# Performance work log

Hardware: AMD Instinct MI355X
Metric: run time of the kernel (lower is better)

Reference implementation:

```python
import jax, jax.numpy as jnp
import numpy as np

N_NODES = 50000
N_EDGES = 800000
F_IN = 512
H1 = 64
H2 = 128
N_CLASSES = 10
N_GRAPHS = 64


def _sage_conv(x, src, dst, w_l, b_l, w_r, n_nodes):
    # mean-aggregate neighbor features (messages flow src -> dst), then
    # out = lin_l(mean_neigh) + lin_r(x)   (PyG SAGEConv defaults)
    msg = x[src]                                           # [E, F] gather
    agg = jax.ops.segment_sum(msg, dst, num_segments=n_nodes)
    deg = jax.ops.segment_sum(jnp.ones((src.shape[0], 1), x.dtype), dst,
                              num_segments=n_nodes)
    mean = agg / jnp.maximum(deg, 1.0)                     # 0 for isolated nodes
    return mean @ w_l + b_l + x @ w_r


def setup_inputs() -> dict:
    key = jax.random.key(0)
    ks = jax.random.split(key, 12)
    x = jax.random.normal(ks[0], (N_NODES, F_IN), dtype=jnp.float32)
    edge_index = jax.random.randint(ks[1], (2, N_EDGES), 0, N_NODES, dtype=jnp.int64)
    batch = jnp.sort(jax.random.randint(ks[2], (N_NODES,), 0, N_GRAPHS, dtype=jnp.int64))

    def glorot(k, fan_in, fan_out):
        s = jnp.sqrt(6.0 / (fan_in + fan_out)).astype(jnp.float32)
        return jax.random.uniform(k, (fan_in, fan_out), jnp.float32, -s, s)

    return {
        "x": x, "edge_index": edge_index, "batch": batch,
        "w1_l": glorot(ks[3], F_IN, H1), "b1_l": jnp.zeros((H1,), jnp.float32),
        "w1_r": glorot(ks[4], F_IN, H1),
        "w2_l": glorot(ks[5], H1, H2), "b2_l": jnp.zeros((H2,), jnp.float32),
        "w2_r": glorot(ks[6], H1, H2),
        "w_fc": glorot(ks[7], H2, N_CLASSES),
        "b_fc": jnp.zeros((N_CLASSES,), jnp.float32),
    }


def reference(x, edge_index, batch, w1_l, b1_l, w1_r, w2_l, b2_l, w2_r, w_fc, b_fc):
    src, dst = edge_index[0], edge_index[1]
    n = x.shape[0]
    h = jax.nn.relu(_sage_conv(x, src, dst, w1_l, b1_l, w1_r, n))
    # dropout is identity in eval mode
    h = _sage_conv(h, src, dst, w2_l, b2_l, w2_r, n)        # [N, H2]
    # global mean pool over graphs
    summed = jax.ops.segment_sum(h, batch, num_segments=N_GRAPHS)
    cnt = jax.ops.segment_sum(jnp.ones((n, 1), h.dtype), batch, num_segments=N_GRAPHS)
    pooled = summed / jnp.maximum(cnt, 1.0)                 # [G, H2]
    logits = pooled @ w_fc + b_fc                           # [G, C]
    return jax.nn.log_softmax(logits, axis=1)
```

## Files before the change

### kernel.cpp

```cpp
#include <hip/hip_runtime.h>

#define NN 50000
#define NE 800000
#define FIN 512
#define H1DIM 64
#define H2DIM 128
#define NC 10
#define NG 64
#define NRT 3125
#define SCAN_BLOCKS 196

typedef __attribute__((ext_vector_type(8))) short bf16x8;
typedef __attribute__((ext_vector_type(4))) float f32x4;

__device__ inline short f2bf(float f) {
  unsigned u = __float_as_uint(f);
  unsigned r = u + 0x7fffu + ((u >> 16) & 1u);
  return (short)(r >> 16);
}
__device__ inline float bf2f(short s) {
  return __uint_as_float(((unsigned)(unsigned short)s) << 16);
}

__global__ __launch_bounds__(256) void hist_kernel(const int* __restrict__ dst,
                                                   int* __restrict__ cnt) {
  int i = (blockIdx.x * 256 + threadIdx.x) * 4;
  if (i < NE) {
    int4 d = *(const int4*)(dst + i);
    atomicAdd(&cnt[d.x], 1);
    atomicAdd(&cnt[d.y], 1);
    atomicAdd(&cnt[d.z], 1);
    atomicAdd(&cnt[d.w], 1);
  }
}

__global__ __launch_bounds__(256) void scan1_kernel(const int* __restrict__ cnt,
                                                    int* __restrict__ excl,
                                                    int* __restrict__ bsum) {
  __shared__ int s[256];
  int t = threadIdx.x;
  int i = blockIdx.x * 256 + t;
  int v = (i < NN) ? cnt[i] : 0;
  s[t] = v;
  __syncthreads();
  for (int off = 1; off < 256; off <<= 1) {
    int u = (t >= off) ? s[t - off] : 0;
    __syncthreads();
    s[t] += u;
    __syncthreads();
  }
  if (i < NN) excl[i] = s[t] - v;
  if (t == 255) bsum[blockIdx.x] = s[255];
}

__global__ __launch_bounds__(256) void scan23_kernel(const int* __restrict__ bsum,
                                                     int* __restrict__ rowptr,
                                                     int* __restrict__ cursor) {
  __shared__ int s[256];
  int t = threadIdx.x;
  int b = blockIdx.x;
  int v = (t < SCAN_BLOCKS) ? bsum[t] : 0;
  s[t] = v;
  __syncthreads();
  for (int off = 1; off < 256; off <<= 1) {
    int u = (t >= off) ? s[t - off] : 0;
    __syncthreads();
    s[t] += u;
    __syncthreads();
  }
  int prefix = (b == 0) ? 0 : s[b - 1];
  int i = b * 256 + t;
  if (i < NN) {
    int p = rowptr[i] + prefix;
    rowptr[i] = p;
    cursor[i] = p;
  }
  if (i == 0) rowptr[NN] = NE;
}

__global__ __launch_bounds__(256) void scatter_kernel(
    const int* __restrict__ src, const int* __restrict__ dst,
    int* __restrict__ cursor, int* __restrict__ ssrc) {
  int i = (blockIdx.x * 256 + threadIdx.x) * 4;
  if (i < NE) {
    int4 s = *(const int4*)(src + i);
    int4 d = *(const int4*)(dst + i);
    int p0 = atomicAdd(&cursor[d.x], 1); ssrc[p0] = s.x;
    int p1 = atomicAdd(&cursor[d.y], 1); ssrc[p1] = s.y;
    int p2 = atomicAdd(&cursor[d.z], 1); ssrc[p2] = s.z;
    int p3 = atomicAdd(&cursor[d.w], 1); ssrc[p3] = s.w;
  }
}

__global__ __launch_bounds__(256) void wbtf_prep_kernel(
    const float* __restrict__ wl, const float* __restrict__ wr,
    short* __restrict__ wbtf) {
  int w = blockIdx.x * 4 + (threadIdx.x >> 6);
  int lane = threadIdx.x & 63;
  int ni = w >> 4;
  int ks = w & 15;
  int n = ni * 16 + (lane & 15);
  int k = ks * 32 + (lane >> 4) * 8;
  bf16x8 o;
#pragma unroll
  for (int j = 0; j < 8; j++) {
    float v = (n < 64) ? wl[(size_t)(k + j) * 64 + n]
                       : wr[(size_t)(k + j) * 64 + (n - 64)];
    o[j] = f2bf(v);
  }
  *(bf16x8*)(wbtf + ((size_t)w * 64 + lane) * 8) = o;
}

__global__ __launch_bounds__(256) void gemm1_kernel(
    const float* __restrict__ x, const short* __restrict__ wbtf,
    short* __restrict__ xwl, float* __restrict__ xwr) {
  int w = blockIdx.x * 4 + (threadIdx.x >> 6);
  if (w >= NRT) return;
  int lane = threadIdx.x & 63;
  int l15 = lane & 15;
  int q = lane >> 4;
  const float* px = x + (size_t)(w * 16 + l15) * FIN + q * 8;
  const short* pb = wbtf + (size_t)lane * 8;

  const f32x4 z = {0.f, 0.f, 0.f, 0.f};
  f32x4 acc[8];
#pragma unroll
  for (int ni = 0; ni < 8; ni++) acc[ni] = z;

  float4 av0, av1, nv0, nv1;
  bf16x8 B0[8], B1[8];
  av0 = *(const float4*)(px);
  av1 = *(const float4*)(px + 4);
#pragma unroll
  for (int ni = 0; ni < 8; ni++)
    B0[ni] = *(const bf16x8*)(pb + (size_t)ni * 8192);

#pragma unroll
  for (int ks = 0; ks < 16; ks += 2) {
    if (ks + 1 < 16) {
      nv0 = *(const float4*)(px + (ks + 1) * 32);
      nv1 = *(const float4*)(px + (ks + 1) * 32 + 4);
#pragma unroll
      for (int ni = 0; ni < 8; ni++)
        B1[ni] = *(const bf16x8*)(pb + (size_t)ni * 8192 + (ks + 1) * 512);
    }
    {
      bf16x8 af;
      af[0] = f2bf(av0.x); af[1] = f2bf(av0.y);
      af[2] = f2bf(av0.z); af[3] = f2bf(av0.w);
      af[4] = f2bf(av1.x); af[5] = f2bf(av1.y);
      af[6] = f2bf(av1.z); af[7] = f2bf(av1.w);
#pragma unroll
      for (int ni = 0; ni < 8; ni++)
        acc[ni] = __builtin_amdgcn_mfma_f32_16x16x32_bf16(af, B0[ni], acc[ni], 0, 0, 0);
    }
    if (ks + 2 < 16) {
      av0 = *(const float4*)(px + (ks + 2) * 32);
      av1 = *(const float4*)(px + (ks + 2) * 32 + 4);
#pragma unroll
      for (int ni = 0; ni < 8; ni++)
        B0[ni] = *(const bf16x8*)(pb + (size_t)ni * 8192 + (ks + 2) * 512);
    }
    {
      bf16x8 af;
      af[0] = f2bf(nv0.x); af[1] = f2bf(nv0.y);
      af[2] = f2bf(nv0.z); af[3] = f2bf(nv0.w);
      af[4] = f2bf(nv1.x); af[5] = f2bf(nv1.y);
      af[6] = f2bf(nv1.z); af[7] = f2bf(nv1.w);
#pragma unroll
      for (int ni = 0; ni < 8; ni++)
        acc[ni] = __builtin_amdgcn_mfma_f32_16x16x32_bf16(af, B1[ni], acc[ni], 0, 0, 0);
    }
  }

  int row_base = w * 16 + q * 4;
#pragma unroll
  for (int ni = 0; ni < 8; ni++) {
    int col = ni * 16 + l15;
    int c = col & 63;
#pragma unroll
    for (int r = 0; r < 4; r++) {
      int row = row_base + r;
      if (col < 64) xwl[(size_t)row * 64 + c] = f2bf(acc[ni][r]);
      else          xwr[(size_t)row * 64 + c] = acc[ni][r];
    }
  }
}

__global__ __launch_bounds__(256) void agg1_h1_kernel(
    const int* __restrict__ rowptr, const int* __restrict__ ssrc,
    const short* __restrict__ xwl, const float* __restrict__ xwr,
    const float* __restrict__ b1, short* __restrict__ h1) {
  int node = blockIdx.x * 4 + (threadIdx.x >> 6);
  if (node >= NN) return;
  int lane = threadIdx.x & 63;
  int c = lane & 7;
  int r = lane >> 3;
  int lo = rowptr[node], hi = rowptr[node + 1];
  float acc[8];
#pragma unroll
  for (int k = 0; k < 8; k++) acc[k] = 0.f;
  for (int e = lo + r; e < hi; e += 8) {
    int s = ssrc[e];
    bf16x8 v = *(const bf16x8*)(xwl + (size_t)s * 64 + c * 8);
#pragma unroll
    for (int k = 0; k < 8; k++) acc[k] += bf2f(v[k]);
  }
#pragma unroll
  for (int k = 0; k < 8; k++) {
    acc[k] += __shfl_xor(acc[k], 8);
    acc[k] += __shfl_xor(acc[k], 16);
    acc[k] += __shfl_xor(acc[k], 32);
  }
  if (r == 0) {
    float dg = fmaxf((float)(hi - lo), 1.0f);
    const float* xr = xwr + (size_t)node * 64 + c * 8;
    bf16x8 out;
#pragma unroll
    for (int k = 0; k < 8; k++) {
      float v = fmaxf(acc[k] / dg + b1[c * 8 + k] + xr[k], 0.f);
      out[k] = f2bf(v);
    }
    *(bf16x8*)(h1 + (size_t)node * 64 + c * 8) = out;
  }
}

__global__ __launch_bounds__(256) void agg2_kernel(
    const int* __restrict__ rowptr, const int* __restrict__ ssrc,
    const short* __restrict__ h1, float* __restrict__ agg2) {
  int node = blockIdx.x * 4 + (threadIdx.x >> 6);
  if (node >= NN) return;
  int lane = threadIdx.x & 63;
  int c = lane & 7;
  int r = lane >> 3;
  int lo = rowptr[node], hi = rowptr[node + 1];
  float acc[8];
#pragma unroll
  for (int k = 0; k < 8; k++) acc[k] = 0.f;
  for (int e = lo + r; e < hi; e += 8) {
    int s = ssrc[e];
    bf16x8 v = *(const bf16x8*)(h1 + (size_t)s * 64 + c * 8);
#pragma unroll
    for (int k = 0; k < 8; k++) acc[k] += bf2f(v[k]);
  }
#pragma unroll
  for (int k = 0; k < 8; k++) {
    acc[k] += __shfl_xor(acc[k], 8);
    acc[k] += __shfl_xor(acc[k], 16);
    acc[k] += __shfl_xor(acc[k], 32);
  }
  if (r == 0) {
    float* p = agg2 + (size_t)node * 64 + c * 8;
    f32x4 lo4 = {acc[0], acc[1], acc[2], acc[3]};
    f32x4 hi4 = {acc[4], acc[5], acc[6], acc[7]};
    *(f32x4*)(p) = lo4;
    *(f32x4*)(p + 4) = hi4;
  }
}

__global__ __launch_bounds__(256) void pool1_kernel(
    const int* __restrict__ batch, const float* __restrict__ agg2,
    const short* __restrict__ h1, const int* __restrict__ rowptr,
    float* __restrict__ poolA, float* __restrict__ poolB,
    float* __restrict__ poolCnt) {
  int t = threadIdx.x;
  int c = t & 15;
  int s = t >> 4;
  int n0 = blockIdx.x * 256 + s * 16;
  int n1 = n0 + 16;
  if (n1 > NN) n1 = NN;

  f32x4 aA = {0.f, 0.f, 0.f, 0.f};
  f32x4 aB = {0.f, 0.f, 0.f, 0.f};
  int cur_g = -1;
  float run = 0.f;
  for (int n = n0; n < n1; n++) {
    int g = batch[n];
    if (g != cur_g) {
      if (cur_g >= 0) {
        float* pa = poolA + (size_t)cur_g * 64 + c * 4;
        float* pb = poolB + (size_t)cur_g * 64 + c * 4;
#pragma unroll
        for (int k = 0; k < 4; k++) {
          atomicAdd(&pa[k], aA[k]);
          atomicAdd(&pb[k], aB[k]);
        }
        if (c == 0) atomicAdd(&poolCnt[cur_g], run);
      }
      cur_g = g;
      aA = (f32x4){0.f, 0.f, 0.f, 0.f};
      aB = (f32x4){0.f, 0.f, 0.f, 0.f};
      run = 0.f;
    }
    float rd = 1.0f / fmaxf((float)(rowptr[n + 1] - rowptr[n]), 1.0f);
    f32x4 a2 = *(const f32x4*)(agg2 + (size_t)n * 64 + c * 4);
    const short* hp = h1 + (size_t)n * 64 + c * 4;
#pragma unroll
    for (int k = 0; k < 4; k++) {
      aA[k] = fmaf(a2[k], rd, aA[k]);
      aB[k] += bf2f(hp[k]);
    }
    run += 1.f;
  }
  if (cur_g >= 0) {
    float* pa = poolA + (size_t)cur_g * 64 + c * 4;
    float* pb = poolB + (size_t)cur_g * 64 + c * 4;
#pragma unroll
    for (int k = 0; k < 4; k++) {
      atomicAdd(&pa[k], aA[k]);
      atomicAdd(&pb[k], aB[k]);
    }
    if (c == 0) atomicAdd(&poolCnt[cur_g], run);
  }
}

__global__ __launch_bounds__(128) void final_kernel(
    const float* __restrict__ poolA, const float* __restrict__ poolB,
    const float* __restrict__ poolCnt, const float* __restrict__ w2l,
    const float* __restrict__ w2r, const float* __restrict__ b2,
    const float* __restrict__ wfc, const float* __restrict__ bfc,
    float* __restrict__ out) {
  int g = blockIdx.x;
  int j = threadIdx.x;
  __shared__ float sp[H2DIM];
  __shared__ float sl[NC];

  float invc = 1.0f / fmaxf(poolCnt[g], 1.0f);
  float v = b2[j];
  for (int k = 0; k < 64; k++) {
    float a = poolA[g * 64 + k] * invc;
    float b = poolB[g * 64 + k] * invc;
    v = fmaf(a, w2l[k * 128 + j], v);
    v = fmaf(b, w2r[k * 128 + j], v);
  }
  sp[j] = v;
  __syncthreads();
  if (j < NC) {
    float lg = bfc[j];
    for (int k = 0; k < H2DIM; k++) lg = fmaf(sp[k], wfc[k * NC + j], lg);
    sl[j] = lg;
  }
  __syncthreads();
  if (j < NC) {
    float m = -1e30f;
    for (int k = 0; k < NC; k++) m = fmaxf(m, sl[k]);
    float s = 0.f;
    for (int k = 0; k < NC; k++) s += expf(sl[k] - m);
    out[g * NC + j] = sl[j] - m - logf(s);
  }
}

extern "C" void kernel_launch(void* const* d_in, const int* in_sizes, int n_in,
                              void* d_out, int out_size, void* d_ws,
                              size_t ws_size, hipStream_t stream) {
  const float* x   = (const float*)d_in[0];
  const int* edge  = (const int*)d_in[1];
  const int* batch = (const int*)d_in[2];
  const float* w1l = (const float*)d_in[3];
  const float* b1l = (const float*)d_in[4];
  const float* w1r = (const float*)d_in[5];
  const float* w2l = (const float*)d_in[6];
  const float* b2l = (const float*)d_in[7];
  const float* w2r = (const float*)d_in[8];
  const float* wfc = (const float*)d_in[9];
  const float* bfc = (const float*)d_in[10];
  float* out = (float*)d_out;

  const int* src = edge;
  const int* dst = edge + NE;

  const size_t NF = (size_t)NN * 64;
  int*   cnt     = (int*)d_ws;
  float* poolA   = (float*)(cnt + NN);
  float* poolB   = poolA + (size_t)NG * 64;
  float* poolCnt = poolB + (size_t)NG * 64;
  int*   cursor  = (int*)(poolCnt + NG);
  int*   rowptr  = cursor + NN;
  int*   bsum    = rowptr + 50004;
  int*   ssrc    = bsum + 256;
  short* xwl     = (short*)(ssrc + NE);
  short* h1s     = xwl + NF;
  short* wbtf    = h1s + NF;
  float* xwr     = (float*)(wbtf + 65536);
  float* agg2    = xwr + NF;

  hipMemsetAsync(cnt, 0, (NN + 2 * NG * 64 + NG) * sizeof(int), stream);

  hist_kernel<<<(NE / 4 + 255) / 256, 256, 0, stream>>>(dst, cnt);
  scan1_kernel<<<SCAN_BLOCKS, 256, 0, stream>>>(cnt, rowptr, bsum);
  scan23_kernel<<<SCAN_BLOCKS, 256, 0, stream>>>(bsum, rowptr, cursor);
  scatter_kernel<<<(NE / 4 + 255) / 256, 256, 0, stream>>>(src, dst, cursor, ssrc);

  wbtf_prep_kernel<<<32, 256, 0, stream>>>(w1l, w1r, wbtf);
  gemm1_kernel<<<(NRT + 3) / 4, 256, 0, stream>>>(x, wbtf, xwl, xwr);

  agg1_h1_kernel<<<(NN + 3) / 4, 256, 0, stream>>>(rowptr, ssrc, xwl, xwr, b1l, h1s);
  agg2_kernel<<<(NN + 3) / 4, 256, 0, stream>>>(rowptr, ssrc, h1s, agg2);
  pool1_kernel<<<SCAN_BLOCKS, 256, 0, stream>>>(batch, agg2, h1s, rowptr, poolA, poolB, poolCnt);
  final_kernel<<<NG, 128, 0, stream>>>(poolA, poolB, poolCnt, w2l, w2r, b2l, wfc, bfc, out);
}
```

Baseline: 381.0 us.

## Stage GEMM1 weights in shared memory and deepen x prefetch

The first-layer GEMM kernel now loads the bf16 weight tile cooperatively into LDS in two halves and shared by the four waves of a block, instead of each wave streaming the full weight matrix from global memory. The x row loads are prefetched four k-steps ahead through a ring of registers. The float-to-bf16 conversion switches to a cheaper round-half-up variant. Out-of-range waves are clamped rather than returned early so they can take part in the block barriers. This adds syncthreads and 64KB of LDS per block, which may limit occupancy, and changes rounding slightly.

Result: faster. 362.7 us (-4.8%).

```diff
diff --git a/kernel.cpp b/kernel.cpp
--- a/kernel.cpp
+++ b/kernel.cpp
@@ -17,6 +17,9 @@
   unsigned u = __float_as_uint(f);
   unsigned r = u + 0x7fffu + ((u >> 16) & 1u);
   return (short)(r >> 16);
+}
+__device__ inline short f2bf_fast(float f) {
+  return (short)((__float_as_uint(f) + 0x8000u) >> 16);
 }
 __device__ inline float bf2f(short s) {
   return __uint_as_float(((unsigned)(unsigned short)s) << 16);
@@ -114,66 +117,66 @@
 __global__ __launch_bounds__(256) void gemm1_kernel(
     const float* __restrict__ x, const short* __restrict__ wbtf,
     short* __restrict__ xwl, float* __restrict__ xwr) {
-  int w = blockIdx.x * 4 + (threadIdx.x >> 6);
-  if (w >= NRT) return;
-  int lane = threadIdx.x & 63;
-  int l15 = lane & 15;
-  int q = lane >> 4;
-  const float* px = x + (size_t)(w * 16 + l15) * FIN + q * 8;
-  const short* pb = wbtf + (size_t)lane * 8;
+  __shared__ short Bs[32768];
+
+  const int t = threadIdx.x;
+  const int w = blockIdx.x * 4 + (t >> 6);
+  const int wc = (w < NRT) ? w : (NRT - 1);
+  const int lane = t & 63;
+  const int l15 = lane & 15;
+  const int q = lane >> 4;
+  const float* px = x + (size_t)(wc * 16 + l15) * FIN + q * 8;
 
   const f32x4 z = {0.f, 0.f, 0.f, 0.f};
   f32x4 acc[8];
 #pragma unroll
   for (int ni = 0; ni < 8; ni++) acc[ni] = z;
 
-  float4 av0, av1, nv0, nv1;
-  bf16x8 B0[8], B1[8];
-  av0 = *(const float4*)(px);
-  av1 = *(const float4*)(px + 4);
-#pragma unroll
-  for (int ni = 0; ni < 8; ni++)
-    B0[ni] = *(const bf16x8*)(pb + (size_t)ni * 8192);
-
-#pragma unroll
-  for (int ks = 0; ks < 16; ks += 2) {
-    if (ks + 1 < 16) {
-      nv0 = *(const float4*)(px + (ks + 1) * 32);
-      nv1 = *(const float4*)(px + (ks + 1) * 32 + 4);
-#pragma unroll
-      for (int ni = 0; ni < 8; ni++)
-        B1[ni] = *(const bf16x8*)(pb + (size_t)ni * 8192 + (ks + 1) * 512);
-    }
-    {
+  float4 ra0[4], ra1[4];
+#pragma unroll
+  for (int i = 0; i < 4; i++) {
+    ra0[i] = *(const float4*)(px + i * 32);
+    ra1[i] = *(const float4*)(px + i * 32 + 4);
+  }
+
+#pragma unroll
+  for (int h = 0; h < 2; h++) {
+    if (h > 0) __syncthreads();
+#pragma unroll
+    for (int i = 0; i < 16; i++) {
+      int c = i * 256 + t;
+      int ni = c >> 9;
+      int rem = c & 511;
+      ((bf16x8*)Bs)[c] =
+          *(const bf16x8*)(wbtf + (size_t)ni * 8192 + h * 4096 + rem * 8);
+    }
+    __syncthreads();
+
+#pragma unroll
+    for (int ksl = 0; ksl < 8; ksl++) {
+      int ks = h * 8 + ksl;
+      int slot = ks & 3;
       bf16x8 af;
-      af[0] = f2bf(av0.x); af[1] = f2bf(av0.y);
-      af[2] = f2bf(av0.z); af[3] = f2bf(av0.w);
-      af[4] = f2bf(av1.x); af[5] = f2bf(av1.y);
-      af[6] = f2bf(av1.z); af[7] = f2bf(av1.w);
-#pragma unroll
-      for (int ni = 0; ni < 8; ni++)
-        acc[ni] = __builtin_amdgcn_mfma_f32_16x16x32_bf16(af, B0[ni], acc[ni], 0, 0, 0);
-    }
-    if (ks + 2 < 16) {
-      av0 = *(const float4*)(px + (ks + 2) * 32);
-      av1 = *(const float4*)(px + (ks + 2) * 32 + 4);
-#pragma unroll
-      for (int ni = 0; ni < 8; ni++)
-        B0[ni] = *(const bf16x8*)(pb + (size_t)ni * 8192 + (ks + 2) * 512);
-    }
-    {
-      bf16x8 af;
-      af[0] = f2bf(nv0.x); af[1] = f2bf(nv0.y);
-      af[2] = f2bf(nv0.z); af[3] = f2bf(nv0.w);
-      af[4] = f2bf(nv1.x); af[5] = f2bf(nv1.y);
-      af[6] = f2bf(nv1.z); af[7] = f2bf(nv1.w);
-#pragma unroll
-      for (int ni = 0; ni < 8; ni++)
-        acc[ni] = __builtin_amdgcn_mfma_f32_16x16x32_bf16(af, B1[ni], acc[ni], 0, 0, 0);
-    }
-  }
-
-  int row_base = w * 16 + q * 4;
+      {
+        float4 v0 = ra0[slot], v1 = ra1[slot];
+        af[0] = f2bf_fast(v0.x); af[1] = f2bf_fast(v0.y);
+        af[2] = f2bf_fast(v0.z); af[3] = f2bf_fast(v0.w);
+        af[4] = f2bf_fast(v1.x); af[5] = f2bf_fast(v1.y);
+        af[6] = f2bf_fast(v1.z); af[7] = f2bf_fast(v1.w);
+      }
+      if (ks + 4 < 16) {
+        ra0[slot] = *(const float4*)(px + (ks + 4) * 32);
+        ra1[slot] = *(const float4*)(px + (ks + 4) * 32 + 4);
+      }
+#pragma unroll
+      for (int ni = 0; ni < 8; ni++) {
+        bf16x8 bf = *(const bf16x8*)(&Bs[((ni * 8 + ksl) * 64 + lane) * 8]);
+        acc[ni] = __builtin_amdgcn_mfma_f32_16x16x32_bf16(af, bf, acc[ni], 0, 0, 0);
+      }
+    }
+  }
+
+  int row_base = wc * 16 + q * 4;
 #pragma unroll
   for (int ni = 0; ni < 8; ni++) {
     int col = ni * 16 + l15;
```
